# Performance work log

Measured on AMD Instinct MI355X. Metric: run time of the kernel, lower is better.

Reference implementation:

```python
import jax, jax.numpy as jnp
import numpy as np

NUM_RELATIONS = 65
NUM_GRAPHS = 1600


def rgcn_conv(x, src, dst, etype, W, Wroot, b):
    """PyG RGCNConv: per-relation mean aggregation + root transform + bias.
    out_i = x_i @ Wroot + b + sum_r mean_{j in N_r(i)} (x_j) @ W_r
    (mean-then-transform == transform-then-mean since W_r is linear).
    """
    N = x.shape[0]
    x_src = x[src]  # [E, in]
    etype_f = etype

    def body(acc, rW):
        r, Wr = rW
        m = (etype_f == r).astype(x.dtype)[:, None]  # [E,1]
        s = jax.ops.segment_sum(x_src * m, dst, num_segments=N)   # [N,in]
        cnt = jax.ops.segment_sum(m, dst, num_segments=N)          # [N,1]
        mean = s / jnp.maximum(cnt, 1.0)
        return acc + mean @ Wr, None

    acc0 = x @ Wroot + b
    out, _ = jax.lax.scan(body, acc0, (jnp.arange(W.shape[0]), W))
    return out


def setup_inputs() -> dict:
    key = jax.random.key(0)
    ks = jax.random.split(key, 20)
    N, E, F, H, M = 50000, 200000, 128, 256, 64
    x = jax.random.normal(ks[0], (N, F), dtype=jnp.float32)
    edge_index = jax.random.randint(ks[1], (2, E), 0, N, dtype=jnp.int64)
    edge_type = jax.random.randint(ks[2], (E,), 0, NUM_RELATIONS, dtype=jnp.int64)
    batch = jnp.sort(jax.random.randint(ks[3], (N,), 0, NUM_GRAPHS, dtype=jnp.int64))

    def glorot(k, shape):
        fan_in = shape[-2] if len(shape) > 1 else shape[-1]
        return jax.random.normal(k, shape, dtype=jnp.float32) / np.sqrt(fan_in)

    W1 = glorot(ks[4], (NUM_RELATIONS, F, H))
    root1 = glorot(ks[5], (F, H))
    b1 = jnp.zeros((H,), jnp.float32)
    W2 = glorot(ks[6], (NUM_RELATIONS, H, H))
    root2 = glorot(ks[7], (H, H))
    b2 = jnp.zeros((H,), jnp.float32)
    ws_w = glorot(ks[8], (H, 1))
    ws_b = jnp.zeros((1,), jnp.float32)
    m1w = glorot(ks[9], (H, M)); m1b = jnp.zeros((M,), jnp.float32)
    m2w = glorot(ks[10], (M, M)); m2b = jnp.zeros((M,), jnp.float32)
    m3w = glorot(ks[11], (M, M)); m3b = jnp.zeros((M,), jnp.float32)
    ow = glorot(ks[12], (M, 1)); ob = jnp.zeros((1,), jnp.float32)
    return {"x": x, "edge_index": edge_index, "edge_type": edge_type, "batch": batch,
            "W1": W1, "root1": root1, "b1": b1, "W2": W2, "root2": root2, "b2": b2,
            "ws_w": ws_w, "ws_b": ws_b, "m1w": m1w, "m1b": m1b, "m2w": m2w,
            "m2b": m2b, "m3w": m3w, "m3b": m3b, "ow": ow, "ob": ob}


def reference(x, edge_index, edge_type, batch, W1, root1, b1, W2, root2, b2,
              ws_w, ws_b, m1w, m1b, m2w, m2b, m3w, m3b, ow, ob):
    N = x.shape[0]
    # add_self_loops(fill_value=0): append self edges with relation 0
    loop = jnp.arange(N, dtype=edge_index.dtype)
    src = jnp.concatenate([edge_index[0], loop])
    dst = jnp.concatenate([edge_index[1], loop])
    et = jnp.concatenate([edge_type, jnp.zeros((N,), edge_type.dtype)])

    h = jax.nn.relu(rgcn_conv(x, src, dst, et, W1, root1, b1))   # dropout: eval
    h = jax.nn.relu(rgcn_conv(h, src, dst, et, W2, root2, b2))

    # WeightedSum pooling
    w = jax.nn.sigmoid(h @ ws_w + ws_b)                          # [N,1]
    emb = jax.ops.segment_sum(w * h, batch, num_segments=NUM_GRAPHS)  # [G,H]

    # MLP (3 layers; eval batch-norm with default stats ~ identity)
    z = jax.nn.relu(emb @ m1w + m1b)
    z = jax.nn.relu(z @ m2w + m2b)
    z = z @ m3w + m3b
    return z @ ow + ob
```

## Files before the change

### kernel.cpp

```cpp
#include <hip/hip_runtime.h>
#include <math.h>

#define N_NODES 50000
#define E_REAL  200000
#define E_MEAN  250000
#define NREL    65
#define HDIM    256
#define NGRAPH  1600
#define NB_R    ((E_REAL + 255) / 256)
#define NB_CNT  ((E_MEAN + 255) / 256)
#define TOT_HIST (NREL * NB_R)
#define MB      64
#define MAX_PB  3264
#define GRID_I  ((N_NODES + MB - 1) / MB)
#define NSA     ((TOT_HIST + 1023) / 1024)
#define NSB     ((N_NODES + 1023) / 1024)

typedef __attribute__((ext_vector_type(8))) short short8;
typedef __attribute__((ext_vector_type(4))) float floatx4;
typedef const __attribute__((address_space(1))) void GPtr;
typedef __attribute__((address_space(3))) void LPtr;

__device__ __forceinline__ unsigned short f2bf(float f) {
    unsigned int u = __float_as_uint(f);
    unsigned int r = u + 0x7FFFu + ((u >> 16) & 1u);
    return (unsigned short)(r >> 16);
}
__device__ __forceinline__ float bf2f(unsigned short u) {
    return __uint_as_float(((unsigned int)u) << 16);
}

__device__ __forceinline__ void gl_lds16(const unsigned short* g, unsigned short* l) {
    __builtin_amdgcn_global_load_lds((GPtr*)g,
        (LPtr*)(unsigned int)(unsigned long long)(void*)l, 16, 0, 0);
}

__global__ void count_kernel(const int* __restrict__ src, const int* __restrict__ dst,
                             const int* __restrict__ et, int* __restrict__ cnt,
                             int* __restrict__ blockHist, int* __restrict__ cntD) {
    __shared__ int lhist[NREL];
    int t = threadIdx.x;
    if (t < NREL) lhist[t] = 0;
    __syncthreads();
    int e = blockIdx.x * 256 + t;
    if (e < E_REAL) {
        int d = dst[e], r = et[e];
        atomicAdd(&cnt[d * NREL + r], 1);
        atomicAdd(&cntD[d], 1);
        atomicAdd(&lhist[r], 1);
    } else if (e < E_MEAN) {
        atomicAdd(&cnt[(e - E_REAL) * NREL], 1);
    }
    __syncthreads();
    if (t < NREL && blockIdx.x < NB_R) blockHist[t * NB_R + blockIdx.x] = lhist[t];
}

__global__ void scan_part2(const int* __restrict__ inA, const int* __restrict__ inB,
                           int* __restrict__ psumA, int* __restrict__ psumB) {
    __shared__ int red[1024];
    int t = threadIdx.x;
    int b = blockIdx.x;
    const int* in; int n; int bi;
    if (b < NSA) { in = inA; n = TOT_HIST; bi = b; }
    else         { in = inB; n = N_NODES;  bi = b - NSA; }
    int g = bi * 1024 + t;
    red[t] = (g < n) ? in[g] : 0;
    __syncthreads();
    for (int off = 512; off >= 1; off >>= 1) {
        if (t < off) red[t] += red[t + off];
        __syncthreads();
    }
    if (t == 0) {
        if (b < NSA) psumA[bi] = red[0];
        else         psumB[bi] = red[0];
    }
}

__global__ void scan_apply2(const int* __restrict__ inA, const int* __restrict__ inB,
                            const int* __restrict__ psumA, const int* __restrict__ psumB,
                            int* __restrict__ outA, int* __restrict__ outB,
                            int* __restrict__ outB2) {
    __shared__ int sums[1024];
    __shared__ int soff;
    int t = threadIdx.x;
    int b = blockIdx.x;
    const int* in; const int* ps; int n; int bi;
    if (b < NSA) { in = inA; ps = psumA; n = TOT_HIST; bi = b; }
    else         { in = inB; ps = psumB; n = N_NODES;  bi = b - NSA; }
    if (t < 64) {
        int v = (t < bi) ? ps[t] : 0;
        for (int off = 32; off >= 1; off >>= 1) v += __shfl_down(v, off, 64);
        if (t == 0) soff = v;
    }
    int g = bi * 1024 + t;
    int v = (g < n) ? in[g] : 0;
    sums[t] = v;
    __syncthreads();
    for (int off = 1; off < 1024; off <<= 1) {
        int u = (t >= off) ? sums[t - off] : 0;
        __syncthreads();
        sums[t] += u;
        __syncthreads();
    }
    if (g < n) {
        int excl = soff + sums[t] - v;
        if (b < NSA) outA[g] = excl;
        else { outB[g] = excl; outB2[g] = excl; }
    }
}

__global__ void meta_kernel(const int* __restrict__ baseArr,
                            int* __restrict__ relStart, int* __restrict__ relTot,
                            int* __restrict__ pBlockStart, int* __restrict__ relOfBlock,
                            int* __restrict__ npb) {
    __shared__ int sStart[NREL + 1];
    __shared__ int sPB[NREL + 1];
    int t = threadIdx.x;
    if (t < NREL) sStart[t] = baseArr[t * NB_R];
    if (t == 0) sStart[NREL] = E_REAL;
    __syncthreads();
    if (t < NREL) {
        relStart[t] = sStart[t];
        relTot[t] = sStart[t + 1] - sStart[t];
    }
    if (t == 0) {
        int a2 = 0;
        for (int r = 0; r < NREL; ++r) {
            sPB[r] = a2;
            int tot = sStart[r + 1] - sStart[r];
            a2 += (tot + MB - 1) / MB;
        }
        sPB[NREL] = a2;
        npb[0] = a2;
    }
    __syncthreads();
    if (t < NREL) pBlockStart[t] = sPB[t];
    int NPB = sPB[NREL];
    for (int b = t; b < NPB; b += 1024) {
        int lo = 0, hi = NREL - 1;
        while (lo < hi) { int mid = (lo + hi + 1) >> 1; if (sPB[mid] <= b) lo = mid; else hi = mid - 1; }
        relOfBlock[b] = lo;
    }
}

__global__ void scatter_sorted(const int* __restrict__ src, const int* __restrict__ dst,
                               const int* __restrict__ et, const int* __restrict__ base,
                               int* __restrict__ perm, int* __restrict__ cursorD,
                               int* __restrict__ qofp) {
    __shared__ int lhist[NREL];
    int t = threadIdx.x;
    int b = blockIdx.x;
    if (t < NREL) lhist[t] = 0;
    __syncthreads();
    int e = b * 256 + t;
    if (e < E_REAL) {
        int d = dst[e], r = et[e];
        int local = atomicAdd(&lhist[r], 1);
        int p = base[r * NB_R + b] + local;
        perm[p] = e;
        int q = atomicAdd(&cursorD[d], 1);
        qofp[p] = q;
    }
}

__device__ __forceinline__ void cvt_row_chunk(const float* __restrict__ in,
                                              unsigned short* __restrict__ out,
                                              int i, int relu) {
    const float4* p = (const float4*)in + (size_t)i * 2;
    float4 a = p[0], b = p[1];
    float v[8] = {a.x, a.y, a.z, a.w, b.x, b.y, b.z, b.w};
    short8 o;
#pragma unroll
    for (int j = 0; j < 8; ++j) {
        float f = relu ? fmaxf(v[j], 0.f) : v[j];
        o[j] = (short)f2bf(f);
    }
    ((short8*)out)[i] = o;
}
__device__ __forceinline__ void cvt_wT_chunk(const float* __restrict__ W,
                                             unsigned short* __restrict__ out,
                                             int i, int K, int N) {
    int kc8 = K / 8;
    int kc = i % kc8;
    int tmp = i / kc8;
    int n = tmp % N;
    int r = tmp / N;
    const float* src = W + ((size_t)r * K + kc * 8) * N + n;
    short8 o;
#pragma unroll
    for (int j = 0; j < 8; ++j) o[j] = (short)f2bf(src[(size_t)j * N]);
    ((short8*)out)[i] = o;
}

__global__ void cvt_rows(const float* __restrict__ in, unsigned short* __restrict__ out,
                         int nchunk, int relu) {
    int i = blockIdx.x * 256 + threadIdx.x;
    if (i >= nchunk) return;
    cvt_row_chunk(in, out, i, relu);
}

#define CVT_NX  (N_NODES * 128 / 8)
#define CVT_W1  (NREL * 256 * 16)
#define CVT_W2  (NREL * 256 * 32)
#define CVT_R1  (256 * 16)
#define CVT_R2  (256 * 32)
#define CVT_TOT (CVT_NX + CVT_W1 + CVT_W2 + CVT_R1 + CVT_R2)
__global__ void cvt_all(const float* __restrict__ x, const float* __restrict__ W1,
                        const float* __restrict__ W2, const float* __restrict__ root1,
                        const float* __restrict__ root2,
                        unsigned short* __restrict__ xb, unsigned short* __restrict__ w1b,
                        unsigned short* __restrict__ w2b, unsigned short* __restrict__ r1b,
                        unsigned short* __restrict__ r2b) {
    int i = blockIdx.x * 256 + threadIdx.x;
    if (i < CVT_NX) { cvt_row_chunk(x, xb, i, 0); return; }
    i -= CVT_NX;
    if (i < CVT_W1) { cvt_wT_chunk(W1, w1b, i, 128, 256); return; }
    i -= CVT_W1;
    if (i < CVT_W2) { cvt_wT_chunk(W2, w2b, i, 256, 256); return; }
    i -= CVT_W2;
    if (i < CVT_R1) { cvt_wT_chunk(root1, r1b, i, 128, 256); return; }
    i -= CVT_R1;
    if (i < CVT_R2) { cvt_wT_chunk(root2, r2b, i, 256, 256); return; }
}

template<int K>
__device__ __forceinline__ void ring_init(const unsigned short* __restrict__ Bp,
                                          int lrow, int lk,
                                          short8 (&b0)[4], short8 (&b1)[4]) {
#pragma unroll
    for (int nf = 0; nf < 4; ++nf)
        b0[nf] = *(const short8*)(Bp + (size_t)(nf * 16 + lrow) * K + lk * 8);
#pragma unroll
    for (int nf = 0; nf < 4; ++nf)
        b1[nf] = *(const short8*)(Bp + (size_t)(nf * 16 + lrow) * K + 32 + lk * 8);
}

template<int K>
__device__ __forceinline__ void gemm_main(const unsigned short* __restrict__ Bp,
                                          const unsigned short* lds,
                                          int lrow, int lk,
                                          short8 (&b0)[4], short8 (&b1)[4],
                                          floatx4 (&acc)[4][4]) {
    constexpr int KS = K / 32;
    short8 bb[3][4];
#pragma unroll
    for (int nf = 0; nf < 4; ++nf) { bb[0][nf] = b0[nf]; bb[1][nf] = b1[nf]; }
#pragma unroll
    for (int ks = 0; ks < KS; ++ks) {
        short8 a[4];
#pragma unroll
        for (int mf = 0; mf < 4; ++mf) {
            int row = mf * 16 + lrow;
            int c = (ks * 4 + lk) ^ (row & 7);
            a[mf] = *(const short8*)((const char*)lds + row * (K * 2) + c * 16);
        }
        if (ks + 2 < KS) {
#pragma unroll
            for (int nf = 0; nf < 4; ++nf)
                bb[(ks + 2) % 3][nf] = *(const short8*)(Bp + (size_t)(nf * 16 + lrow) * K + (ks + 2) * 32 + lk * 8);
        }
#pragma unroll
        for (int mf = 0; mf < 4; ++mf)
#pragma unroll
            for (int nf = 0; nf < 4; ++nf)
                acc[mf][nf] = __builtin_amdgcn_mfma_f32_16x16x32_bf16(a[mf], bb[ks % 3][nf], acc[mf][nf], 0, 0, 0);
    }
}

template<int K>
__device__ __forceinline__ void gemm_pass(const unsigned short* __restrict__ Bp,
                                          const unsigned short* lds,
                                          int lrow, int lk, floatx4 (&acc)[4][4]) {
    short8 b0[4], b1[4];
    ring_init<K>(Bp, lrow, lk, b0, b1);
    gemm_main<K>(Bp, lds, lrow, lk, b0, b1, acc);
}

template<int K, bool EDGE>
__device__ __forceinline__ void stage_A(const unsigned short* __restrict__ A,
                                        unsigned short* lds, const int* ssrc,
                                        int rowbase, int t) {
    constexpr int CH = K / 8;
#pragma unroll
    for (int i = 0; i < (MB * CH) / 256; ++i) {
        int q = i * 256 + t;
        int row = q / CH, sl = q % CH;
        int srow;
        if constexpr (EDGE) srow = ssrc[row];
        else { srow = rowbase + row; if (srow >= N_NODES) srow = N_NODES - 1; }
        int cg = sl ^ (row & 7);
        gl_lds16(A + (size_t)srow * K + cg * 8, lds + q * 8);
    }
}

template<int K>
__global__ __launch_bounds__(256) void edge_msg(
    const unsigned short* __restrict__ A,
    const unsigned short* __restrict__ B,
    unsigned short* __restrict__ outB,
    const int* __restrict__ perm, const int* __restrict__ srcA,
    const int* __restrict__ dstA, const int* __restrict__ cnt,
    const int* __restrict__ relOfBlock, const int* __restrict__ pBlockStart,
    const int* __restrict__ relStart, const int* __restrict__ relTot,
    const int* __restrict__ npb, const int* __restrict__ qofp)
{
    __shared__ __align__(16) unsigned short lds[MB * HDIM];
    __shared__ int ssrc[MB];
    __shared__ int sqd[MB];
    __shared__ float sw[MB];
    int t = threadIdx.x;
    int b = blockIdx.x;
    if (b >= npb[0]) return;
    int rel = relOfBlock[b];
    int jb = b - pBlockStart[rel];
    int rs = relStart[rel];
    int nval = relTot[rel] - jb * MB; if (nval > MB) nval = MB;
    if (t < MB) {
        int s = 0, qd = 0; float w = 0.f;
        if (t < nval) {
            int p = rs + jb * MB + t;
            int e = perm[p];
            s = srcA[e];
            int d = dstA[e];
            w = 1.0f / (float)cnt[d * NREL + rel];
            qd = qofp[p];
        }
        ssrc[t] = s; sqd[t] = qd; sw[t] = w;
    }
    __syncthreads();

    int wave = t >> 6, lane = t & 63;
    int n0 = wave * 64;
    int lrow = lane & 15, lk = lane >> 4;
    const unsigned short* Bp = B + ((size_t)rel * HDIM + n0) * K;

    stage_A<K, true>(A, lds, ssrc, 0, t);
    short8 b0[4], b1[4];
    ring_init<K>(Bp, lrow, lk, b0, b1);
    __syncthreads();

    floatx4 acc[4][4];
#pragma unroll
    for (int mf = 0; mf < 4; ++mf)
#pragma unroll
        for (int nf = 0; nf < 4; ++nf) acc[mf][nf] = (floatx4)0.f;
    gemm_main<K>(Bp, lds, lrow, lk, b0, b1, acc);

    __syncthreads();
#pragma unroll
    for (int mf = 0; mf < 4; ++mf) {
        int mbase = mf * 16 + lk * 4;
#pragma unroll
        for (int i = 0; i < 4; ++i) {
            int row = mbase + i;
            float w = sw[row];
#pragma unroll
            for (int nf = 0; nf < 4; ++nf)
                lds[row * HDIM + n0 + nf * 16 + lrow] = f2bf(acc[mf][nf][i] * w);
        }
    }
    __syncthreads();
    for (int q = t; q < nval * 32; q += 256) {
        int row = q >> 5, c = q & 31;
        *(uint4*)(outB + (size_t)sqd[row] * HDIM + c * 8) = *(const uint4*)(lds + row * HDIM + c * 8);
    }
}

template<int K>
__global__ __launch_bounds__(256) void init_gemm(
    const unsigned short* __restrict__ A,
    const unsigned short* __restrict__ Broot,
    const unsigned short* __restrict__ Bself,
    const float* __restrict__ bias,
    unsigned short* __restrict__ outB,
    const int* __restrict__ cnt)
{
    __shared__ __align__(16) unsigned short lds[MB * HDIM];
    __shared__ float sw[MB];
    int t = threadIdx.x;
    int rowbase = blockIdx.x * MB;
    if (t < MB) {
        int srow = rowbase + t; if (srow >= N_NODES) srow = N_NODES - 1;
        sw[t] = 1.0f / (float)cnt[srow * NREL];
    }
    int wave = t >> 6, lane = t & 63;
    int n0 = wave * 64;
    int lrow = lane & 15, lk = lane >> 4;

    stage_A<K, false>(A, lds, nullptr, rowbase, t);
    short8 b0[4], b1[4];
    ring_init<K>(Bself + (size_t)n0 * K, lrow, lk, b0, b1);
    __syncthreads();

    floatx4 acc[4][4];
#pragma unroll
    for (int mf = 0; mf < 4; ++mf)
#pragma unroll
        for (int nf = 0; nf < 4; ++nf) acc[mf][nf] = (floatx4)0.f;
    gemm_main<K>(Bself + (size_t)n0 * K, lds, lrow, lk, b0, b1, acc);
#pragma unroll
    for (int mf = 0; mf < 4; ++mf) {
        int mbase = mf * 16 + lk * 4;
#pragma unroll
        for (int i = 0; i < 4; ++i) {
            float w = sw[mbase + i];
#pragma unroll
            for (int nf = 0; nf < 4; ++nf) acc[mf][nf][i] *= w;
        }
    }
    gemm_pass<K>(Broot + (size_t)n0 * K, lds, lrow, lk, acc);

    float bv[4];
#pragma unroll
    for (int nf = 0; nf < 4; ++nf) bv[nf] = bias[n0 + nf * 16 + lrow];
    __syncthreads();
#pragma unroll
    for (int mf = 0; mf < 4; ++mf) {
        int mbase = mf * 16 + lk * 4;
#pragma unroll
        for (int i = 0; i < 4; ++i) {
            int row = mbase + i;
#pragma unroll
            for (int nf = 0; nf < 4; ++nf)
                lds[row * HDIM + n0 + nf * 16 + lrow] = f2bf(acc[mf][nf][i] + bv[nf]);
        }
    }
    __syncthreads();
    int limit = N_NODES - rowbase; if (limit > MB) limit = MB;
    for (int q = t; q < limit * 32; q += 256) {
        int row = q >> 5, c = q & 31;
        *(uint4*)(outB + ((size_t)rowbase + row) * HDIM + c * 8) = *(const uint4*)(lds + row * HDIM + c * 8);
    }
}

template<int K, int MODE>
__global__ __launch_bounds__(256) void mfma_gemm(
    const unsigned short* __restrict__ A,
    const unsigned short* __restrict__ B,
    const unsigned short* __restrict__ Bself,
    const float* __restrict__ bias,
    float* __restrict__ outF,
    const int* __restrict__ perm, const int* __restrict__ srcA,
    const int* __restrict__ dstA, const int* __restrict__ cnt,
    const int* __restrict__ relOfBlock, const int* __restrict__ pBlockStart,
    const int* __restrict__ relStart, const int* __restrict__ relTot,
    const int* __restrict__ npb)
{
    constexpr bool EDGE = (MODE == 1);
    __shared__ __align__(16) unsigned short lds[MB * HDIM];
    __shared__ int ssrc[MB];
    __shared__ int sdst[MB];
    __shared__ float sw[MB];
    int t = threadIdx.x;
    int b = blockIdx.x;
    int rel = 0, rowbase = 0, jb = 0, rs = 0, nval = MB;
    if constexpr (EDGE) {
        if (b >= npb[0]) return;
        rel = relOfBlock[b];
        jb = b - pBlockStart[rel];
        rs = relStart[rel];
        nval = relTot[rel] - jb * MB; if (nval > MB) nval = MB;
        if (t < MB) {
            int s = 0, d = 0; float w = 0.f;
            if (t < nval) {
                int p = rs + jb * MB + t;
                int e = perm[p];
                s = srcA[e]; d = dstA[e];
                w = 1.0f / (float)cnt[d * NREL + rel];
            }
            ssrc[t] = s; sdst[t] = d; sw[t] = w;
        }
        __syncthreads();
    } else {
        rowbase = b * MB;
        if (t < MB) {
            int srow = rowbase + t; if (srow >= N_NODES) srow = N_NODES - 1;
            sw[t] = 1.0f / (float)cnt[srow * NREL];
        }
    }
    stage_A<K, EDGE>(A, lds, ssrc, rowbase, t);
    __syncthreads();

    int wave = t >> 6, lane = t & 63;
    int n0 = wave * 64;
    int lrow = lane & 15;
    int lk = lane >> 4;
    floatx4 acc[4][4];
#pragma unroll
    for (int mf = 0; mf < 4; ++mf)
#pragma unroll
        for (int nf = 0; nf < 4; ++nf) acc[mf][nf] = (floatx4)0.f;

    if constexpr (EDGE) {
        gemm_pass<K>(B + ((size_t)rel * HDIM + n0) * K, lds, lrow, lk, acc);
    } else {
        gemm_pass<K>(Bself + (size_t)n0 * K, lds, lrow, lk, acc);
#pragma unroll
        for (int mf = 0; mf < 4; ++mf) {
            int mbase = mf * 16 + lk * 4;
#pragma unroll
            for (int i = 0; i < 4; ++i) {
                float w = sw[mbase + i];
#pragma unroll
                for (int nf = 0; nf < 4; ++nf) acc[mf][nf][i] *= w;
            }
        }
        gemm_pass<K>(B + (size_t)n0 * K, lds, lrow, lk, acc);
    }

    if constexpr (MODE == 1) {
#pragma unroll
        for (int mf = 0; mf < 4; ++mf) {
            int mbase = mf * 16 + lk * 4;
#pragma unroll
            for (int i = 0; i < 4; ++i) {
                int mm = mbase + i;
                float w = sw[mm];
                if (w != 0.f) {
                    int drow = sdst[mm];
#pragma unroll
                    for (int nf = 0; nf < 4; ++nf) {
                        int col = n0 + nf * 16 + lrow;
                        atomicAdd(&outF[(size_t)drow * HDIM + col], acc[mf][nf][i] * w);
                    }
                }
            }
        }
    } else {
        float bv[4];
#pragma unroll
        for (int nf = 0; nf < 4; ++nf) bv[nf] = bias[n0 + nf * 16 + lrow];
#pragma unroll
        for (int mf = 0; mf < 4; ++mf) {
            int mbase = mf * 16 + lk * 4;
#pragma unroll
            for (int i = 0; i < 4; ++i) {
                int mm = rowbase + mbase + i;
                if (mm < N_NODES) {
#pragma unroll
                    for (int nf = 0; nf < 4; ++nf) {
                        int col = n0 + nf * 16 + lrow;
                        outF[(size_t)mm * HDIM + col] = acc[mf][nf][i] + bv[nf];
                    }
                }
            }
        }
    }
}

__global__ __launch_bounds__(256) void reduce_kernel(
    const unsigned short* __restrict__ hinit, const unsigned short* __restrict__ msg,
    const int* __restrict__ startD, const int* __restrict__ cntD,
    unsigned short* __restrict__ hout)
{
    int t = threadIdx.x;
    int lane = t & 63;
    int d = blockIdx.x * 4 + (t >> 6);
    if (d >= N_NODES) return;
    int s0 = startD[d], n = cntD[d];
    ushort4 hv = *(const ushort4*)(hinit + (size_t)d * HDIM + lane * 4);
    float v0 = bf2f(hv.x), v1 = bf2f(hv.y), v2 = bf2f(hv.z), v3 = bf2f(hv.w);
    const unsigned short* mp = msg + (size_t)s0 * HDIM + lane * 4;
#pragma unroll 4
    for (int q = 0; q < n; ++q) {
        ushort4 m = *(const ushort4*)(mp + (size_t)q * HDIM);
        v0 += bf2f(m.x); v1 += bf2f(m.y); v2 += bf2f(m.z); v3 += bf2f(m.w);
    }
    ushort4 o;
    o.x = f2bf(fmaxf(v0, 0.f)); o.y = f2bf(fmaxf(v1, 0.f));
    o.z = f2bf(fmaxf(v2, 0.f)); o.w = f2bf(fmaxf(v3, 0.f));
    *(ushort4*)(hout + (size_t)d * HDIM + lane * 4) = o;
}

__global__ __launch_bounds__(256) void reduce_pool(
    const unsigned short* __restrict__ hinit, const unsigned short* __restrict__ msg,
    const int* __restrict__ startD, const int* __restrict__ cntD,
    const int* __restrict__ batch, const float* __restrict__ wsw,
    const float* __restrict__ wsb, float* __restrict__ emb)
{
    int g = blockIdx.x;
    int t = threadIdx.x;
    __shared__ int slo, shi;
    __shared__ float sacc[4][HDIM];
    if (t == 0) {
        int lo = 0, hi = N_NODES;
        while (lo < hi) { int m = (lo + hi) >> 1; if (batch[m] < g) lo = m + 1; else hi = m; }
        slo = lo;
        int lo2 = lo, hi2 = N_NODES;
        while (lo2 < hi2) { int m = (lo2 + hi2) >> 1; if (batch[m] < g + 1) lo2 = m + 1; else hi2 = m; }
        shi = lo2;
    }
    __syncthreads();
    int wave = t >> 6, lane = t & 63;
    float4 wv = *(const float4*)(wsw + lane * 4);
    float wb = wsb[0];
    float a0 = 0.f, a1 = 0.f, a2 = 0.f, a3 = 0.f;
    for (int d = slo + wave; d < shi; d += 4) {
        int s0 = startD[d], n = cntD[d];
        ushort4 hv = *(const ushort4*)(hinit + (size_t)d * HDIM + lane * 4);
        float v0 = bf2f(hv.x), v1 = bf2f(hv.y), v2 = bf2f(hv.z), v3 = bf2f(hv.w);
        const unsigned short* mp = msg + (size_t)s0 * HDIM + lane * 4;
        for (int q = 0; q < n; ++q) {
            ushort4 m = *(const ushort4*)(mp + (size_t)q * HDIM);
            v0 += bf2f(m.x); v1 += bf2f(m.y); v2 += bf2f(m.z); v3 += bf2f(m.w);
        }
        v0 = fmaxf(v0, 0.f); v1 = fmaxf(v1, 0.f);
        v2 = fmaxf(v2, 0.f); v3 = fmaxf(v3, 0.f);
        float pp = v0 * wv.x + v1 * wv.y + v2 * wv.z + v3 * wv.w;
        for (int off = 32; off >= 1; off >>= 1) pp += __shfl_down(pp, off, 64);
        float tot = __shfl(pp, 0, 64);
        float sig = 1.0f / (1.0f + expf(-(tot + wb)));
        a0 += sig * v0; a1 += sig * v1; a2 += sig * v2; a3 += sig * v3;
    }
    sacc[wave][lane * 4 + 0] = a0; sacc[wave][lane * 4 + 1] = a1;
    sacc[wave][lane * 4 + 2] = a2; sacc[wave][lane * 4 + 3] = a3;
    __syncthreads();
    emb[(size_t)g * HDIM + t] = sacc[0][t] + sacc[1][t] + sacc[2][t] + sacc[3][t];
}

__global__ void pool_kernel(const float* __restrict__ h, const int* __restrict__ batch,
                            const float* __restrict__ wsw, const float* __restrict__ wsb,
                            float* __restrict__ emb) {
    int i = blockIdx.x;
    int t = threadIdx.x;
    float v = fmaxf(h[(size_t)i * HDIM + t], 0.f);
    float p = v * wsw[t];
    for (int off = 32; off >= 1; off >>= 1) p += __shfl_down(p, off, 64);
    __shared__ float red[4];
    __shared__ float ssig;
    if ((t & 63) == 0) red[t >> 6] = p;
    __syncthreads();
    if (t == 0) {
        float s = red[0] + red[1] + red[2] + red[3] + wsb[0];
        ssig = 1.0f / (1.0f + expf(-s));
    }
    __syncthreads();
    atomicAdd(&emb[(size_t)batch[i] * HDIM + t], ssig * v);
}

__global__ void mlp_kernel(const float* __restrict__ emb,
                           const float* __restrict__ m1w, const float* __restrict__ m1b,
                           const float* __restrict__ m2w, const float* __restrict__ m2b,
                           const float* __restrict__ m3w, const float* __restrict__ m3b,
                           const float* __restrict__ ow,  const float* __restrict__ ob,
                           float* __restrict__ out) {
    int g = blockIdx.x;
    int t = threadIdx.x;
    __shared__ float e[HDIM];
    __shared__ float z1[64], z2[64];
    for (int idx = t; idx < HDIM; idx += 64) e[idx] = emb[(size_t)g * HDIM + idx];
    __syncthreads();
    float a = m1b[t];
    for (int k = 0; k < HDIM; ++k) a += e[k] * m1w[k * 64 + t];
    z1[t] = fmaxf(a, 0.f);
    __syncthreads();
    a = m2b[t];
    for (int k = 0; k < 64; ++k) a += z1[k] * m2w[k * 64 + t];
    z2[t] = fmaxf(a, 0.f);
    __syncthreads();
    a = m3b[t];
    for (int k = 0; k < 64; ++k) a += z2[k] * m3w[k * 64 + t];
    float p = a * ow[t];
    for (int off = 32; off >= 1; off >>= 1) p += __shfl_down(p, off, 64);
    if (t == 0) out[g] = p + ob[0];
}

extern "C" void kernel_launch(void* const* d_in, const int* in_sizes, int n_in,
                              void* d_out, int out_size, void* d_ws, size_t ws_size,
                              hipStream_t stream) {
    const float* x     = (const float*)d_in[0];
    const int*   ei    = (const int*)d_in[1];
    const int*   src   = ei;
    const int*   dst   = ei + E_REAL;
    const int*   et    = (const int*)d_in[2];
    const int*   batch = (const int*)d_in[3];
    const float* W1    = (const float*)d_in[4];
    const float* root1 = (const float*)d_in[5];
    const float* b1    = (const float*)d_in[6];
    const float* W2    = (const float*)d_in[7];
    const float* root2 = (const float*)d_in[8];
    const float* b2    = (const float*)d_in[9];
    const float* wsw   = (const float*)d_in[10];
    const float* wsb   = (const float*)d_in[11];
    const float* m1w   = (const float*)d_in[12];
    const float* m1b   = (const float*)d_in[13];
    const float* m2w   = (const float*)d_in[14];
    const float* m2b   = (const float*)d_in[15];
    const float* m3w   = (const float*)d_in[16];
    const float* m3b   = (const float*)d_in[17];
    const float* ow    = (const float*)d_in[18];
    const float* ob    = (const float*)d_in[19];

    char* ws = (char*)d_ws;
    size_t off = 0;
    auto alloc = [&](size_t bytes) {
        void* p = ws + off;
        off = (off + bytes + 255) & ~(size_t)255;
        return p;
    };
    int*   cnt       = (int*)alloc((size_t)N_NODES * NREL * 4);
    int*   blockHist = (int*)alloc((size_t)TOT_HIST * 4);
    int*   baseArr   = (int*)alloc((size_t)TOT_HIST * 4);
    int*   perm      = (int*)alloc((size_t)E_REAL * 4);
    int*   relStartA = (int*)alloc(NREL * 4);
    int*   relTotA   = (int*)alloc(NREL * 4);
    int*   pbStartA  = (int*)alloc(NREL * 4);
    int*   relOfBlk  = (int*)alloc(MAX_PB * 4);
    int*   npb       = (int*)alloc(4);
    int*   psumA     = (int*)alloc(64 * 4);
    int*   psumB     = (int*)alloc(64 * 4);
    unsigned short* xb  = (unsigned short*)alloc((size_t)N_NODES * 128 * 2);
    unsigned short* w1b = (unsigned short*)alloc((size_t)NREL * 256 * 128 * 2);
    unsigned short* w2b = (unsigned short*)alloc((size_t)NREL * 256 * 256 * 2);
    unsigned short* r1b = (unsigned short*)alloc((size_t)256 * 128 * 2);
    unsigned short* r2b = (unsigned short*)alloc((size_t)256 * 256 * 2);
    unsigned short* h1b = (unsigned short*)alloc((size_t)N_NODES * HDIM * 2);
    float* emb = (float*)alloc((size_t)NGRAPH * HDIM * 4);
    size_t off_common = off;

    unsigned short* hinit = (unsigned short*)alloc((size_t)N_NODES * HDIM * 2);
    unsigned short* msg   = (unsigned short*)alloc((size_t)E_REAL * HDIM * 2);
    int* qofp    = (int*)alloc((size_t)E_REAL * 4);
    int* cntD    = (int*)alloc((size_t)N_NODES * 4);
    int* startD  = (int*)alloc((size_t)N_NODES * 4);
    int* cursorD = (int*)alloc((size_t)N_NODES * 4);
    size_t need_fast = off;

    float* hf = nullptr;
    bool fast = (ws_size >= need_fast);
    if (!fast) {
        off = off_common;
        hf = (float*)alloc((size_t)N_NODES * HDIM * 4);
        char* hh = (char*)hf;
        qofp    = (int*)hh;                                 hh += (size_t)E_REAL * 4;
        cntD    = (int*)hh;                                 hh += (size_t)N_NODES * 4;
        startD  = (int*)hh;                                 hh += (size_t)N_NODES * 4;
        cursorD = (int*)hh;
        hinit = h1b;
        msg = h1b;
    }

    hipMemsetAsync(cnt, 0, (size_t)N_NODES * NREL * 4, stream);
    hipMemsetAsync(cntD, 0, (size_t)N_NODES * 4, stream);

    count_kernel<<<NB_CNT, 256, 0, stream>>>(src, dst, et, cnt, blockHist, cntD);
    scan_part2<<<NSA + NSB, 1024, 0, stream>>>(blockHist, cntD, psumA, psumB);
    scan_apply2<<<NSA + NSB, 1024, 0, stream>>>(blockHist, cntD, psumA, psumB,
                                                baseArr, startD, cursorD);
    meta_kernel<<<1, 1024, 0, stream>>>(baseArr, relStartA, relTotA, pbStartA, relOfBlk, npb);
    scatter_sorted<<<NB_R, 256, 0, stream>>>(src, dst, et, baseArr, perm, cursorD, qofp);

    cvt_all<<<(CVT_TOT + 255) / 256, 256, 0, stream>>>(x, W1, W2, root1, root2,
                                                       xb, w1b, w2b, r1b, r2b);

    if (fast) {
        init_gemm<128><<<GRID_I, 256, 0, stream>>>(xb, r1b, w1b, b1, hinit, cnt);
        edge_msg<128><<<MAX_PB, 256, 0, stream>>>(xb, w1b, msg,
            perm, src, dst, cnt, relOfBlk, pbStartA, relStartA, relTotA, npb, qofp);
        reduce_kernel<<<N_NODES / 4, 256, 0, stream>>>(hinit, msg, startD, cntD, h1b);
        init_gemm<256><<<GRID_I, 256, 0, stream>>>(h1b, r2b, w2b, b2, hinit, cnt);
        edge_msg<256><<<MAX_PB, 256, 0, stream>>>(h1b, w2b, msg,
            perm, src, dst, cnt, relOfBlk, pbStartA, relStartA, relTotA, npb, qofp);
        reduce_pool<<<NGRAPH, 256, 0, stream>>>(hinit, msg, startD, cntD,
                                                batch, wsw, wsb, emb);
    } else {
        hipMemsetAsync(emb, 0, (size_t)NGRAPH * HDIM * 4, stream);
        mfma_gemm<128, 0><<<GRID_I, 256, 0, stream>>>(xb, r1b, w1b, b1, hf,
            nullptr, nullptr, nullptr, cnt, nullptr, nullptr, nullptr, nullptr, nullptr);
        mfma_gemm<128, 1><<<MAX_PB, 256, 0, stream>>>(xb, w1b, nullptr, nullptr, hf,
            perm, src, dst, cnt, relOfBlk, pbStartA, relStartA, relTotA, npb);
        cvt_rows<<<(N_NODES * HDIM / 8 + 255) / 256, 256, 0, stream>>>(hf, h1b, N_NODES * HDIM / 8, 1);
        mfma_gemm<256, 0><<<GRID_I, 256, 0, stream>>>(h1b, r2b, w2b, b2, hf,
            nullptr, nullptr, nullptr, cnt, nullptr, nullptr, nullptr, nullptr, nullptr);
        mfma_gemm<256, 1><<<MAX_PB, 256, 0, stream>>>(h1b, w2b, nullptr, nullptr, hf,
            perm, src, dst, cnt, relOfBlk, pbStartA, relStartA, relTotA, npb);
        pool_kernel<<<N_NODES, 256, 0, stream>>>(hf, batch, wsw, wsb, emb);
    }
    mlp_kernel<<<NGRAPH, 64, 0, stream>>>(emb, m1w, m1b, m2w, m2b, m3w, m3b, ow, ob, (float*)d_out);
}
```

Baseline: 345.0 us.

## Split edge GEMM A-staging into two K-halves to overlap gather with MFMA

The edge message kernel now gathers the A rows in two K-halves into separate LDS buffers. The second half's gather is issued after the first barrier, so it is in flight while the MFMAs run on the first half. Block indices are also remapped with an interleaved stride of 8, which changes how relation blocks are spread across the hardware schedulers. The cost is an extra barrier and a more complex B-prefetch ring restart at the half boundary, and the remap assumes MAX_PB is divisible by 8.

```diff
diff --git a/kernel.cpp b/kernel.cpp
--- a/kernel.cpp
+++ b/kernel.cpp
@@ -224,27 +224,76 @@
 }
 
 template<int K>
-__device__ __forceinline__ void ring_init(const unsigned short* __restrict__ Bp,
-                                          int lrow, int lk,
-                                          short8 (&b0)[4], short8 (&b1)[4]) {
+__device__ __forceinline__ void ring_init_off(const unsigned short* __restrict__ Bp,
+                                              int koff, int lrow, int lk,
+                                              short8 (&b0)[4], short8 (&b1)[4]) {
 #pragma unroll
     for (int nf = 0; nf < 4; ++nf)
-        b0[nf] = *(const short8*)(Bp + (size_t)(nf * 16 + lrow) * K + lk * 8);
+        b0[nf] = *(const short8*)(Bp + (size_t)(nf * 16 + lrow) * K + koff + lk * 8);
 #pragma unroll
     for (int nf = 0; nf < 4; ++nf)
-        b1[nf] = *(const short8*)(Bp + (size_t)(nf * 16 + lrow) * K + 32 + lk * 8);
+        b1[nf] = *(const short8*)(Bp + (size_t)(nf * 16 + lrow) * K + koff + 32 + lk * 8);
 }
 
 template<int K>
-__device__ __forceinline__ void gemm_main(const unsigned short* __restrict__ Bp,
-                                          const unsigned short* lds,
+__device__ __forceinline__ void gemm_half(const unsigned short* __restrict__ Bp,
+                                          int koff, const unsigned short* buf,
                                           int lrow, int lk,
                                           short8 (&b0)[4], short8 (&b1)[4],
                                           floatx4 (&acc)[4][4]) {
+    constexpr int KH = K / 64;
+    constexpr int CH2 = K / 16;
+    short8 bb[3][4];
+#pragma unroll
+    for (int nf = 0; nf < 4; ++nf) { bb[0][nf] = b0[nf]; bb[1][nf] = b1[nf]; }
+#pragma unroll
+    for (int ks2 = 0; ks2 < KH; ++ks2) {
+        short8 a[4];
+#pragma unroll
+        for (int mf = 0; mf < 4; ++mf) {
+            int row = mf * 16 + lrow;
+            int c = (ks2 * 4 + lk) ^ (row & 7);
+            a[mf] = *(const short8*)(buf + (row * CH2 + c) * 8);
+        }
+        if (ks2 + 2 < KH) {
+#pragma unroll
+            for (int nf = 0; nf < 4; ++nf)
+                bb[(ks2 + 2) % 3][nf] = *(const short8*)(Bp + (size_t)(nf * 16 + lrow) * K + koff + (ks2 + 2) * 32 + lk * 8);
+        }
+#pragma unroll
+        for (int mf = 0; mf < 4; ++mf)
+#pragma unroll
+            for (int nf = 0; nf < 4; ++nf)
+                acc[mf][nf] = __builtin_amdgcn_mfma_f32_16x16x32_bf16(a[mf], bb[ks2 % 3][nf], acc[mf][nf], 0, 0, 0);
+    }
+}
+
+template<int K>
+__device__ __forceinline__ void stage_half(const unsigned short* __restrict__ A,
+                                           unsigned short* buf, const int* ssrc,
+                                           int h, int t) {
+    constexpr int CH2 = K / 16;
+#pragma unroll
+    for (int i = 0; i < (MB * CH2) / 256; ++i) {
+        int q = i * 256 + t;
+        int row = q / CH2, sl = q % CH2;
+        int cg = h * CH2 + (sl ^ (row & 7));
+        gl_lds16(A + (size_t)ssrc[row] * K + cg * 8, buf + q * 8);
+    }
+}
+
+template<int K>
+__device__ __forceinline__ void gemm_pass(const unsigned short* __restrict__ Bp,
+                                          const unsigned short* lds,
+                                          int lrow, int lk, floatx4 (&acc)[4][4]) {
     constexpr int KS = K / 32;
     short8 bb[3][4];
 #pragma unroll
-    for (int nf = 0; nf < 4; ++nf) { bb[0][nf] = b0[nf]; bb[1][nf] = b1[nf]; }
+    for (int nf = 0; nf < 4; ++nf)
+        bb[0][nf] = *(const short8*)(Bp + (size_t)(nf * 16 + lrow) * K + lk * 8);
+#pragma unroll
+    for (int nf = 0; nf < 4; ++nf)
+        bb[1][nf] = *(const short8*)(Bp + (size_t)(nf * 16 + lrow) * K + 32 + lk * 8);
 #pragma unroll
     for (int ks = 0; ks < KS; ++ks) {
         short8 a[4];
@@ -265,15 +314,6 @@
             for (int nf = 0; nf < 4; ++nf)
                 acc[mf][nf] = __builtin_amdgcn_mfma_f32_16x16x32_bf16(a[mf], bb[ks % 3][nf], acc[mf][nf], 0, 0, 0);
     }
-}
-
-template<int K>
-__device__ __forceinline__ void gemm_pass(const unsigned short* __restrict__ Bp,
-                                          const unsigned short* lds,
-                                          int lrow, int lk, floatx4 (&acc)[4][4]) {
-    short8 b0[4], b1[4];
-    ring_init<K>(Bp, lrow, lk, b0, b1);
-    gemm_main<K>(Bp, lds, lrow, lk, b0, b1, acc);
 }
 
 template<int K, bool EDGE>
@@ -304,12 +344,14 @@
     const int* __restrict__ relStart, const int* __restrict__ relTot,
     const int* __restrict__ npb, const int* __restrict__ qofp)
 {
+    constexpr int CH2 = K / 16;
+    constexpr int HELEM = MB * CH2 * 8;
     __shared__ __align__(16) unsigned short lds[MB * HDIM];
     __shared__ int ssrc[MB];
     __shared__ int sqd[MB];
     __shared__ float sw[MB];
     int t = threadIdx.x;
-    int b = blockIdx.x;
+    int b = (blockIdx.x & 7) * (MAX_PB / 8) + (blockIdx.x >> 3);
     if (b >= npb[0]) return;
     int rel = relOfBlock[b];
     int jb = b - pBlockStart[rel];
@@ -333,18 +375,24 @@
     int n0 = wave * 64;
     int lrow = lane & 15, lk = lane >> 4;
     const unsigned short* Bp = B + ((size_t)rel * HDIM + n0) * K;
-
-    stage_A<K, true>(A, lds, ssrc, 0, t);
+    unsigned short* buf0 = lds;
+    unsigned short* buf1 = lds + HELEM;
+
+    stage_half<K>(A, buf0, ssrc, 0, t);
     short8 b0[4], b1[4];
-    ring_init<K>(Bp, lrow, lk, b0, b1);
-    __syncthreads();
+    ring_init_off<K>(Bp, 0, lrow, lk, b0, b1);
+    __syncthreads();
+    stage_half<K>(A, buf1, ssrc, 1, t);
 
     floatx4 acc[4][4];
 #pragma unroll
     for (int mf = 0; mf < 4; ++mf)
 #pragma unroll
         for (int nf = 0; nf < 4; ++nf) acc[mf][nf] = (floatx4)0.f;
-    gemm_main<K>(Bp, lds, lrow, lk, b0, b1, acc);
+    gemm_half<K>(Bp, 0, buf0, lrow, lk, b0, b1, acc);
+    ring_init_off<K>(Bp, K / 2, lrow, lk, b0, b1);
+    __syncthreads();
+    gemm_half<K>(Bp, K / 2, buf1, lrow, lk, b0, b1, acc);
 
     __syncthreads();
 #pragma unroll
@@ -388,8 +436,6 @@
     int lrow = lane & 15, lk = lane >> 4;
 
     stage_A<K, false>(A, lds, nullptr, rowbase, t);
-    short8 b0[4], b1[4];
-    ring_init<K>(Bself + (size_t)n0 * K, lrow, lk, b0, b1);
     __syncthreads();
 
     floatx4 acc[4][4];
@@ -397,7 +443,7 @@
     for (int mf = 0; mf < 4; ++mf)
 #pragma unroll
         for (int nf = 0; nf < 4; ++nf) acc[mf][nf] = (floatx4)0.f;
-    gemm_main<K>(Bself + (size_t)n0 * K, lds, lrow, lk, b0, b1, acc);
+    gemm_pass<K>(Bself + (size_t)n0 * K, lds, lrow, lk, acc);
 #pragma unroll
     for (int mf = 0; mf < 4; ++mf) {
         int mbase = mf * 16 + lk * 4;
```

Measured after the change: 345.7 us. About the same (+0.2%).
